# Optimization experiments

Measured on AMD Instinct MI355X. Metric: run time of the kernel, lower is better.

Reference implementation:

```python
import jax, jax.numpy as jnp
import numpy as np
import math

B, S, D, H = 2, 2048, 1024, 16
DK = D // H
EPS = 1e-5

def setup_inputs() -> dict:
    key = jax.random.key(0)
    ks = jax.random.split(key, 16)
    s = 0.02
    return {
        'query': jax.random.normal(ks[0], (B, S, D), jnp.float32),
        'key': jax.random.normal(ks[1], (B, S, D), jnp.float32),
        'value': jax.random.normal(ks[2], (B, S, D), jnp.float32),
        'mask': jax.random.randint(ks[3], (B, 1, S, S), 0, 2, jnp.int32),
        'market_context': jax.random.normal(ks[4], (B, D), jnp.float32),
        'Wq': jax.random.normal(ks[5], (D, D), jnp.float32) * s,
        'bq': jnp.zeros((D,), jnp.float32),
        'Wk': jax.random.normal(ks[6], (D, D), jnp.float32) * s,
        'bk': jnp.zeros((D,), jnp.float32),
        'Wv': jax.random.normal(ks[7], (D, D), jnp.float32) * s,
        'bv': jnp.zeros((D,), jnp.float32),
        'Wo': jax.random.normal(ks[8], (D, D), jnp.float32) * s,
        'bo': jnp.zeros((D,), jnp.float32),
        'Wc': jax.random.normal(ks[9], (D, D), jnp.float32) * s,
        'bc': jnp.zeros((D,), jnp.float32),
        'ln_g': jnp.ones((D,), jnp.float32),
        'ln_b': jnp.zeros((D,), jnp.float32),
    }

def reference(query, key, value, mask, market_context,
              Wq, bq, Wk, bk, Wv, bv, Wo, bo, Wc, bc, ln_g, ln_b):
    b, s, d = query.shape
    # QKV projections -> [B, H, S, DK]
    Q = (query @ Wq + bq).reshape(b, s, H, DK).transpose(0, 2, 1, 3)
    K = (key @ Wk + bk).reshape(b, s, H, DK).transpose(0, 2, 1, 3)
    V = (value @ Wv + bv).reshape(b, s, H, DK).transpose(0, 2, 1, 3)
    # market context -> per-head bias added to K (broadcast over sequence)
    ctx = (market_context @ Wc + bc).reshape(b, H, DK)
    K = K + ctx[:, :, None, :]
    scores = jnp.einsum('bhqd,bhkd->bhqk', Q, K) / math.sqrt(DK)
    scores = jnp.where(mask == 0, jnp.float32(-1e9), scores)
    attn = jax.nn.softmax(scores, axis=-1)  # dropout is identity in eval
    ctx2 = jnp.einsum('bhqk,bhkd->bhqd', attn, V)
    ctx2 = ctx2.transpose(0, 2, 1, 3).reshape(b, s, d)
    out = ctx2 @ Wo + bo
    x = out + query
    mu = jnp.mean(x, axis=-1, keepdims=True)
    var = jnp.mean((x - mu) ** 2, axis=-1, keepdims=True)
    return (x - mu) * jax.lax.rsqrt(var + EPS) * ln_g + ln_b
```

## Files before the change

### kernel.cpp

```cpp
#include <hip/hip_runtime.h>
#include <cstdint>

typedef unsigned short u16;
typedef __attribute__((ext_vector_type(8))) short s16x8;
typedef __attribute__((ext_vector_type(8))) unsigned short u16x8;
typedef __attribute__((ext_vector_type(4))) float f32x4;
typedef __attribute__((ext_vector_type(16))) float f32x16;
typedef __attribute__((ext_vector_type(2))) unsigned uint2v;
typedef __attribute__((ext_vector_type(4))) unsigned uint4v;

#define CKF 0.18033688011f

__device__ inline u16 f2bf(float f){
  union { float f; uint32_t u; } v; v.f = f;
  uint32_t r = v.u + 0x7fffu + ((v.u >> 16) & 1u);
  return (u16)(r >> 16);
}

__device__ inline f32x4 mfma16(s16x8 a, s16x8 b, f32x4 c){
  return __builtin_amdgcn_mfma_f32_16x16x32_bf16(a, b, c, 0, 0, 0);
}
__device__ inline f32x16 mfma32(s16x8 a, s16x8 b, f32x16 c){
  return __builtin_amdgcn_mfma_f32_32x32x16_bf16(a, b, c, 0, 0, 0);
}
__device__ inline unsigned cvtpk(float a, float b){
  unsigned r;
  asm("v_cvt_pk_bf16_f32 %0, %1, %2" : "=v"(r) : "v"(a), "v"(b));
  return r;
}
__device__ inline float exp2a(float x){
  float r;
  asm("v_exp_f32 %0, %1" : "=v"(r) : "v"(x));
  return r;
}
__device__ inline void glds16(const u16* g, u16* l){
  __builtin_amdgcn_global_load_lds((const __attribute__((address_space(1))) void*)g,
                                   (__attribute__((address_space(3))) void*)l, 16, 0, 0);
}
__device__ inline void glds4(const unsigned* g, unsigned* l){
  __builtin_amdgcn_global_load_lds((const __attribute__((address_space(1))) void*)g,
                                   (__attribute__((address_space(3))) void*)l, 4, 0, 0);
}

__global__ __launch_bounds__(256) void convert3_kernel(
    const float* __restrict__ q, const float* __restrict__ k, const float* __restrict__ v,
    u16* __restrict__ qo, u16* __restrict__ ko, u16* __restrict__ vo){
  const float* src = (blockIdx.y == 0) ? q : (blockIdx.y == 1) ? k : v;
  u16* dst = (blockIdx.y == 0) ? qo : (blockIdx.y == 1) ? ko : vo;
  size_t i = ((size_t)blockIdx.x * 256 + threadIdx.x) * 8;
  float4 a = *(const float4*)(src + i);
  float4 b = *(const float4*)(src + i + 4);
  u16x8 o = { f2bf(a.x), f2bf(a.y), f2bf(a.z), f2bf(a.w),
              f2bf(b.x), f2bf(b.y), f2bf(b.z), f2bf(b.w) };
  *(u16x8*)(dst + i) = o;
}

__global__ void transw_kernel(
    const float* __restrict__ W0, const float* __restrict__ W1,
    const float* __restrict__ W2, const float* __restrict__ W3,
    u16* __restrict__ T0, u16* __restrict__ T1, u16* __restrict__ T2, u16* __restrict__ T3){
  const float* W = (blockIdx.z == 0) ? W0 : (blockIdx.z == 1) ? W1 : (blockIdx.z == 2) ? W2 : W3;
  u16* T = (blockIdx.z == 0) ? T0 : (blockIdx.z == 1) ? T1 : (blockIdx.z == 2) ? T2 : T3;
  __shared__ float t[32][33];
  int n0 = blockIdx.x * 32, k0 = blockIdx.y * 32;
  int tx = threadIdx.x, ty = threadIdx.y;
  #pragma unroll
  for (int j = 0; j < 4; j++)
    t[ty + j*8][tx] = W[(size_t)(k0 + ty + j*8) * 1024 + n0 + tx];
  __syncthreads();
  #pragma unroll
  for (int j = 0; j < 4; j++)
    T[(size_t)(n0 + ty + j*8) * 1024 + k0 + tx] = f2bf(t[tx][ty + j*8]);
}

__global__ __launch_bounds__(256) void packmask_kernel(const int* __restrict__ mask,
                                                       unsigned* __restrict__ bits){
  size_t i = (size_t)blockIdx.x * 256 + threadIdx.x;
  int v = mask[i];
  unsigned long long bal = __ballot(v != 0);
  int lane = threadIdx.x & 63;
  if (lane == 0)       bits[i >> 5] = (unsigned)bal;
  else if (lane == 32) bits[i >> 5] = (unsigned)(bal >> 32);
}

__global__ __launch_bounds__(256) void ctx_kernel(const float* __restrict__ mc,
                                                  const float* __restrict__ Wc,
                                                  const float* __restrict__ bc,
                                                  float* __restrict__ ctx){
  int c = threadIdx.x & 63, kk = threadIdx.x >> 6;
  int col = blockIdx.x * 64 + c;
  float a0 = 0.f, a1 = 0.f;
  for (int k = kk * 256; k < kk * 256 + 256; k++){
    float wv = Wc[(size_t)k * 1024 + col];
    a0 += mc[k] * wv;
    a1 += mc[1024 + k] * wv;
  }
  __shared__ float red[2][4][64];
  red[0][kk][c] = a0; red[1][kk][c] = a1;
  __syncthreads();
  if (threadIdx.x < 64){
    int cc = threadIdx.x;
    ctx[blockIdx.x*64 + cc] = red[0][0][cc] + red[0][1][cc] + red[0][2][cc] + red[0][3][cc]
                              + bc[blockIdx.x*64 + cc];
  } else if (threadIdx.x < 128){
    int cc = threadIdx.x - 64;
    ctx[1024 + blockIdx.x*64 + cc] = red[1][0][cc] + red[1][1][cc] + red[1][2][cc] + red[1][3][cc]
                                     + bc[blockIdx.x*64 + cc];
  }
}

struct GemmParams {
  const u16* A0; const u16* A1; const u16* A2; const u16* A3;
  const u16* W0; const u16* W1; const u16* W2; const u16* W3;
  const float* b0; const float* b1; const float* b2;
  const float* ctx;
  u16* outQ; u16* outK; u16* outV; float* outX0; float* outX1;
  int which;
};

__global__ __launch_bounds__(256) void gemm_kernel(GemmParams P){
  int o = blockIdx.x + (blockIdx.y << 3) + (blockIdx.z << 8);
  int xcd = o & 7, j = o >> 3;
  int by = xcd + ((j & 3) << 3);
  int bx = (j >> 2) & 7;
  int bz = j >> 5;

  int z, kbase, nkt;
  const u16* A; const u16* W;
  if (P.which < 0){
    z = bz; kbase = 0; nkt = 32;
    if (z == 0){ A = P.A0; W = P.W0; }
    else if (z == 1){ A = P.A1; W = P.W1; }
    else { A = P.A2; W = P.W2; }
  } else {
    z = 3; kbase = bz * 512; nkt = 16;
    A = P.A3; W = P.W3;
  }
  int m0 = by * 128, n0 = bx * 128;
  __shared__ __align__(16) u16 sm[16384];
  int tid = threadIdx.x, lane = tid & 63, w = tid >> 6;
  int li = lane & 15, lq = lane >> 4;
  int wm = w >> 1, wn = w & 1;
  f32x4 zero = {0.f, 0.f, 0.f, 0.f};
  f32x4 acc[4][4];
  #pragma unroll
  for (int i = 0; i < 4; i++)
    #pragma unroll
    for (int jj = 0; jj < 4; jj++) acc[i][jj] = zero;

  int scolS = ((lane & 3) ^ ((lane >> 3) & 3)) << 3;
  int row0 = w * 16 + (lane >> 2);
  const u16* aS0 = A + (size_t)(m0 + row0) * 1024 + kbase + scolS;
  const u16* aS1 = aS0 + (size_t)64 * 1024;
  const u16* bS0 = W + (size_t)(n0 + row0) * 1024 + kbase + scolS;
  const u16* bS1 = bS0 + (size_t)64 * 1024;
  int aD0 = (w * 64) * 8, aD1 = (256 + w * 64) * 8;

  int aOff[4], bOff[4];
  #pragma unroll
  for (int mb = 0; mb < 4; mb++){
    int row = wm * 64 + mb * 16 + li;
    aOff[mb] = (row * 32 + ((lq ^ ((row >> 1) & 3)) << 3)) * 2;
  }
  #pragma unroll
  for (int nb = 0; nb < 4; nb++){
    int row = wn * 64 + nb * 16 + li;
    bOff[nb] = 8192 + (row * 32 + ((lq ^ ((row >> 1) & 3)) << 3)) * 2;
  }

  auto STAGE = [&](int ct){
    u16* Ab = &sm[ct * 8192];
    u16* Bb = &sm[ct * 8192 + 4096];
    glds16(aS0, Ab + aD0);
    glds16(aS1, Ab + aD1);
    glds16(bS0, Bb + aD0);
    glds16(bS1, Bb + aD1);
  };
  auto ADV = [&](){ aS0 += 32; aS1 += 32; bS0 += 32; bS1 += 32; };

  auto KITER = [&](int kt, int ct){
    __builtin_amdgcn_s_barrier();
    if (kt + 1 < nkt){
      STAGE(ct ^ 1); ADV();
      asm volatile("s_waitcnt vmcnt(4)" ::: "memory");
    } else {
      asm volatile("s_waitcnt vmcnt(0)" ::: "memory");
    }
    __builtin_amdgcn_sched_barrier(0);
    __builtin_amdgcn_s_barrier();
    const char* base = (const char*)sm + ct * 16384;
    s16x8 af[4], bfr[4];
    #pragma unroll
    for (int mb = 0; mb < 4; mb++) af[mb] = *(const s16x8*)(base + aOff[mb]);
    #pragma unroll
    for (int nb = 0; nb < 4; nb++) bfr[nb] = *(const s16x8*)(base + bOff[nb]);
    __builtin_amdgcn_s_setprio(1);
    #pragma unroll
    for (int mb = 0; mb < 4; mb++)
      #pragma unroll
      for (int nb = 0; nb < 4; nb++)
        acc[mb][nb] = mfma16(af[mb], bfr[nb], acc[mb][nb]);
    __builtin_amdgcn_s_setprio(0);
  };

  STAGE(0); ADV();
  for (int kt = 0; kt < nkt; kt += 2){
    KITER(kt, 0);
    KITER(kt + 1, 1);
  }

  if (z == 2){
    const float* bias = P.b2;
    __syncthreads();
    u16* Ot = sm;
    #pragma unroll
    for (int mb = 0; mb < 4; mb++){
      #pragma unroll
      for (int nb = 0; nb < 4; nb++){
        int colL = wn * 64 + nb * 16 + li;
        int rowB = wm * 64 + mb * 16 + lq * 4;
        float bcol = bias[n0 + colL];
        unsigned p01 = cvtpk(acc[mb][nb][0] + bcol, acc[mb][nb][1] + bcol);
        unsigned p23 = cvtpk(acc[mb][nb][2] + bcol, acc[mb][nb][3] + bcol);
        int ba = colL * 256 + ((rowB * 2) ^ ((colL & 7) << 4));
        *(unsigned*)((char*)Ot + ba) = p01;
        *(unsigned*)((char*)Ot + ba + 4) = p23;
      }
    }
    __syncthreads();
    int bq_ = m0 >> 11, srow0 = m0 & 2047;
    #pragma unroll
    for (int i = 0; i < 8; i++){
      int u = i * 256 + tid;
      int colL = u >> 4, sc = u & 15;
      int ba = colL * 256 + ((sc * 16) ^ ((colL & 7) << 4));
      u16x8 vv = *(const u16x8*)((char*)Ot + ba);
      *(u16x8*)(P.outV + (((size_t)(bq_ * 1024 + n0 + colL)) << 11) + srow0 + sc * 8) = vv;
    }
    return;
  }

  if (z == 3){
    float* Xo = (kbase == 0) ? P.outX0 : P.outX1;
    #pragma unroll
    for (int mb = 0; mb < 4; mb++){
      #pragma unroll
      for (int nb = 0; nb < 4; nb++){
        int col = n0 + wn * 64 + nb * 16 + li;
        #pragma unroll
        for (int r = 0; r < 4; r++){
          int row = m0 + wm * 64 + mb * 16 + lq * 4 + r;
          Xo[(size_t)row * 1024 + col] = acc[mb][nb][r];
        }
      }
    }
    return;
  }

  const float* bias = (z == 0) ? P.b0 : P.b1;
  #pragma unroll
  for (int mb = 0; mb < 4; mb++){
    #pragma unroll
    for (int nb = 0; nb < 4; nb++){
      int colL = wn * 64 + nb * 16 + li; int col = n0 + colL;
      float bcol = bias[col];
      #pragma unroll
      for (int r = 0; r < 4; r++){
        int row = m0 + wm * 64 + mb * 16 + lq * 4 + r;
        float v = acc[mb][nb][r] + bcol;
        if (z == 0){
          P.outQ[(size_t)row * 1024 + col] = f2bf(v * CKF);
        } else {
          v += P.ctx[(size_t)(row >> 11) * 1024 + col];
          P.outK[(size_t)row * 1024 + col] = f2bf(v);
        }
      }
    }
  }
}

__global__ __launch_bounds__(256) void attn_kernel(
    const u16* __restrict__ Qg, const u16* __restrict__ Kg, const u16* __restrict__ Vtg,
    const unsigned* __restrict__ mbits, u16* __restrict__ ctx2){
  __shared__ __align__(16) u16 arena[17408];
  int tid = threadIdx.x, lane = tid & 63, w = tid >> 6;
  int l31 = lane & 31, hi = lane >> 5;
  int r7 = l31 & 7;
  int orig = blockIdx.x + (blockIdx.y << 4);
  int swz = (orig & 7) * 64 + (orig >> 3);
  int q0 = (swz & 15) * 128, bh = swz >> 4, b = bh >> 4, h = bh & 15;

  s16x8 qf[4];
  {
    const u16* qp = Qg + (size_t)(b * 2048 + q0 + w * 32 + l31) * 1024 + h * 64 + hi * 8;
    #pragma unroll
    for (int ks = 0; ks < 4; ks++)
      qf[ks] = *(const s16x8*)(qp + ks * 16);
  }
  s16x8 onesf;
  #pragma unroll
  for (int e = 0; e < 8; e++) onesf[e] = (short)0x3F80;
  f32x16 ZERO;
  #pragma unroll
  for (int r = 0; r < 16; r++) ZERO[r] = 0.f;

  int scolS = ((lane & 7) ^ (lane >> 3)) << 3;
  int rowS = w * 16 + (lane >> 3);
  const u16* kS0 = Kg + (size_t)(b * 2048 + rowS) * 1024 + h * 64 + scolS;
  const u16* kS1 = kS0 + (size_t)8 * 1024;
  const u16* vS0 = Vtg + (((size_t)(bh * 64 + rowS)) << 11) + scolS;
  const u16* vS1 = vS0 + ((size_t)8 << 11);
  int um = w * 64 + lane;
  const unsigned* mS = mbits + (size_t)(b * 2048 + q0 + (um >> 1)) * 64 + (um & 1);
  int kD0 = w * 1024, kD1 = w * 1024 + 512;

  int qr = w * 32 + l31;
  int koff[2][4], voff[2][4];
  #pragma unroll
  for (int jj = 0; jj < 2; jj++)
    #pragma unroll
    for (int ks = 0; ks < 4; ks++){
      koff[jj][ks] = ((jj * 32 + l31) * 64 + (((ks * 2 + hi) ^ r7) << 3)) * 2;
      voff[jj][ks] = 8192 + ((jj * 32 + l31) * 64 + (((ks * 2 + hi) ^ r7) << 3)) * 2;
    }
  int mB = 32768 + qr * 8;

  auto STAGE = [&](int ct){
    u16* dst = &arena[ct * 8192];
    glds16(kS0, dst + kD0);
    glds16(kS1, dst + kD1);
    glds16(vS0, dst + 4096 + kD0);
    glds16(vS1, dst + 4096 + kD1);
    glds4(mS, (unsigned*)&arena[16384] + ct * 256 + w * 64);
  };
  auto ADV = [&](){
    kS0 += (size_t)64 * 1024; kS1 += (size_t)64 * 1024;
    vS0 += 64; vS1 += 64; mS += 2;
  };

  f32x16 accO[2], accS;
  #pragma unroll
  for (int d = 0; d < 2; d++) accO[d] = ZERO;
  accS = ZERO;

  STAGE(0); ADV();

  auto ITER = [&](int t, int ct){
    __builtin_amdgcn_s_barrier();
    if (t < 31){
      STAGE(ct ^ 1); ADV();
      asm volatile("s_waitcnt vmcnt(5)" ::: "memory");
    } else {
      asm volatile("s_waitcnt vmcnt(0)" ::: "memory");
    }
    __builtin_amdgcn_sched_barrier(0);
    __builtin_amdgcn_s_barrier();
    const char* base = (const char*)arena + ct * 16384;

    f32x16 S[2];
    __builtin_amdgcn_s_setprio(1);
    #pragma unroll
    for (int jj = 0; jj < 2; jj++){
      S[jj] = ZERO;
      #pragma unroll
      for (int ks = 0; ks < 4; ks++){
        s16x8 kf = *(const s16x8*)(base + koff[jj][ks]);
        S[jj] = mfma32(kf, qf[ks], S[jj]);
      }
    }
    __builtin_amdgcn_s_setprio(0);

    uint2v mw = *(const uint2v*)((const char*)arena + ct * 1024 + mB);
    unsigned mh0 = mw[0] >> (hi << 2), mh1 = mw[1] >> (hi << 2);
    #pragma unroll
    for (int jj = 0; jj < 2; jj++){
      unsigned mh = jj ? mh1 : mh0;
      #pragma unroll
      for (int rg = 0; rg < 16; rg++){
        int pos = (rg & 3) + ((rg >> 2) << 3);
        float pv = exp2a(S[jj][rg]);
        S[jj][rg] = ((mh >> pos) & 1u) ? pv : 0.f;
      }
    }

    s16x8 pf[4];
    #pragma unroll
    for (int jj = 0; jj < 2; jj++){
      #pragma unroll
      for (int hs = 0; hs < 2; hs++){
        int rb = hs * 8;
        unsigned A0 = cvtpk(S[jj][rb + 0], S[jj][rb + 1]);
        unsigned A1 = cvtpk(S[jj][rb + 2], S[jj][rb + 3]);
        unsigned B0 = cvtpk(S[jj][rb + 4], S[jj][rb + 5]);
        unsigned B1 = cvtpk(S[jj][rb + 6], S[jj][rb + 7]);
        uint2v r01 = __builtin_amdgcn_permlane32_swap(A0, B0, false, false);
        uint2v r23 = __builtin_amdgcn_permlane32_swap(A1, B1, false, false);
        uint4v uu = { r01[0], r23[0], r01[1], r23[1] };
        pf[jj * 2 + hs] = *(s16x8*)&uu;
      }
    }
    __builtin_amdgcn_s_setprio(1);
    #pragma unroll
    for (int c = 0; c < 4; c++){
      #pragma unroll
      for (int dh = 0; dh < 2; dh++){
        s16x8 vf = *(const s16x8*)(base + voff[dh][c]);
        accO[dh] = mfma32(vf, pf[c], accO[dh]);
      }
      accS = mfma32(onesf, pf[c], accS);
    }
    __builtin_amdgcn_s_setprio(0);
  };

  for (int t = 0; t < 32; t += 2){
    ITER(t, 0);
    ITER(t + 1, 1);
  }

  __syncthreads();
  float lsum = accS[0];
  float inv = 1.f / lsum;
  u16* Ot = arena;
  #pragma unroll
  for (int dh = 0; dh < 2; dh++){
    #pragma unroll
    for (int rg = 0; rg < 16; rg += 2){
      int dk = dh * 32 + (rg & 3) + ((rg >> 2) << 3) + (hi << 2);
      unsigned pk = cvtpk(accO[dh][rg] * inv, accO[dh][rg + 1] * inv);
      *(unsigned*)&Ot[qr * 64 + (((dk >> 3) ^ (qr & 7)) << 3) + (dk & 7)] = pk;
    }
  }
  __syncthreads();
  #pragma unroll
  for (int i = 0; i < 4; i++){
    int u = i * 256 + tid, row = u >> 3, slot = u & 7;
    u16x8 vv = *(const u16x8*)&Ot[row * 64 + ((slot ^ (row & 7)) << 3)];
    *(u16x8*)(ctx2 + (size_t)(b * 2048 + q0 + row) * 1024 + h * 64 + slot * 8) = vv;
  }
}

__global__ __launch_bounds__(256) void ln_kernel(const float* __restrict__ X0,
                                                 const float* __restrict__ X1,
                                                 const float* __restrict__ qres,
                                                 const float* __restrict__ bo,
                                                 const float* __restrict__ g,
                                                 const float* __restrict__ bb,
                                                 float* __restrict__ out){
  size_t row = blockIdx.x;
  int tid = threadIdx.x;
  float4 a = *(const float4*)(X0 + row * 1024 + tid * 4);
  float4 c = *(const float4*)(X1 + row * 1024 + tid * 4);
  float4 q = *(const float4*)(qres + row * 1024 + tid * 4);
  float4 bv = *(const float4*)(bo + tid * 4);
  float4 v;
  v.x = a.x + c.x + q.x + bv.x;
  v.y = a.y + c.y + q.y + bv.y;
  v.z = a.z + c.z + q.z + bv.z;
  v.w = a.w + c.w + q.w + bv.w;
  float s = v.x + v.y + v.z + v.w;
  float s2 = v.x*v.x + v.y*v.y + v.z*v.z + v.w*v.w;
  #pragma unroll
  for (int o = 1; o < 64; o <<= 1){
    s += __shfl_xor(s, o, 64);
    s2 += __shfl_xor(s2, o, 64);
  }
  __shared__ float rs[4], rs2[4];
  int w = tid >> 6;
  if ((tid & 63) == 0){ rs[w] = s; rs2[w] = s2; }
  __syncthreads();
  s = rs[0] + rs[1] + rs[2] + rs[3];
  s2 = rs2[0] + rs2[1] + rs2[2] + rs2[3];
  float mu = s * (1.f / 1024.f);
  float var = s2 * (1.f / 1024.f) - mu * mu;
  float rstd = rsqrtf(var + 1e-5f);
  float4 gg = *(const float4*)(g + tid * 4);
  float4 bt = *(const float4*)(bb + tid * 4);
  float4 o;
  o.x = (v.x - mu) * rstd * gg.x + bt.x;
  o.y = (v.y - mu) * rstd * gg.y + bt.y;
  o.z = (v.z - mu) * rstd * gg.z + bt.z;
  o.w = (v.w - mu) * rstd * gg.w + bt.w;
  *(float4*)(out + row * 1024 + tid * 4) = o;
}

extern "C" void kernel_launch(void* const* d_in, const int* in_sizes, int n_in,
                              void* d_out, int out_size, void* d_ws, size_t ws_size,
                              hipStream_t stream){
  const float* query = (const float*)d_in[0];
  const float* key_  = (const float*)d_in[1];
  const float* value = (const float*)d_in[2];
  const int*   mask  = (const int*)d_in[3];
  const float* mc    = (const float*)d_in[4];
  const float* Wq = (const float*)d_in[5];  const float* bq = (const float*)d_in[6];
  const float* Wk = (const float*)d_in[7];  const float* bk = (const float*)d_in[8];
  const float* Wv = (const float*)d_in[9];  const float* bv = (const float*)d_in[10];
  const float* Wo = (const float*)d_in[11]; const float* bo = (const float*)d_in[12];
  const float* Wc = (const float*)d_in[13]; const float* bc = (const float*)d_in[14];
  const float* lng = (const float*)d_in[15]; const float* lnb = (const float*)d_in[16];
  float* outp = (float*)d_out;
  uint8_t* ws = (uint8_t*)d_ws;
  const size_t MB = (size_t)1 << 20;
  if (ws_size < 58 * MB) return;

  u16* q_bf = (u16*)(ws + 0);
  u16* k_bf = (u16*)(ws + 8 * MB);
  u16* v_bf = (u16*)(ws + 16 * MB);
  float* X0 = (float*)(ws + 8 * MB);
  u16* Qb   = (u16*)(ws + 24 * MB);
  u16* Kb   = (u16*)(ws + 32 * MB);
  float* X1 = (float*)(ws + 32 * MB);
  u16* Vt   = (u16*)(ws + 40 * MB);
  u16* Wqt  = (u16*)(ws + 48 * MB);
  u16* Wkt  = (u16*)(ws + 50 * MB);
  u16* Wvt  = (u16*)(ws + 52 * MB);
  u16* Wot  = (u16*)(ws + 54 * MB);
  unsigned* mbits = (unsigned*)(ws + 56 * MB);
  float* ctxf = (float*)(ws + 57 * MB);
  u16* ctx2 = q_bf;

  convert3_kernel<<<dim3(2048, 3), 256, 0, stream>>>(query, key_, value, q_bf, k_bf, v_bf);
  transw_kernel<<<dim3(32, 32, 4), dim3(32, 8), 0, stream>>>(Wq, Wk, Wv, Wo, Wqt, Wkt, Wvt, Wot);
  packmask_kernel<<<32768, 256, 0, stream>>>(mask, mbits);
  ctx_kernel<<<16, 256, 0, stream>>>(mc, Wc, bc, ctxf);

  GemmParams gp;
  gp.A0 = q_bf; gp.A1 = k_bf; gp.A2 = v_bf; gp.A3 = ctx2;
  gp.W0 = Wqt;  gp.W1 = Wkt;  gp.W2 = Wvt;  gp.W3 = Wot;
  gp.b0 = bq;   gp.b1 = bk;   gp.b2 = bv;
  gp.ctx = ctxf;
  gp.outQ = Qb; gp.outK = Kb; gp.outV = Vt; gp.outX0 = X0; gp.outX1 = X1;
  gp.which = -1;
  gemm_kernel<<<dim3(8, 32, 3), 256, 0, stream>>>(gp);

  attn_kernel<<<dim3(16, 32), 256, 0, stream>>>(Qb, Kb, Vt, mbits, ctx2);

  gp.which = 3;
  gemm_kernel<<<dim3(8, 32, 2), 256, 0, stream>>>(gp);

  ln_kernel<<<4096, 256, 0, stream>>>(X0, X1, query, bo, lng, lnb, outp);
}
```

Before: 170.1 us.

## Merge prep kernels into one launch and widen GEMM tiles to 128x256

Four preprocessing kernels (input conversion, weight transpose, mask packing, context projection) are merged into a single launch that dispatches on block index, which removes three launch gaps. The GEMM tile grows from 128x128 to 128x256 with 8 accumulator fragments per wave, more shared memory and launch_bounds(256,2). The V-transpose epilogue now runs in two halves so it fits the shared buffer. This gives more operand reuse per tile, at the cost of half as many blocks (fewer than the CU count for the output projection) and higher register pressure.

```diff
diff --git a/kernel.cpp b/kernel.cpp
--- a/kernel.cpp
+++ b/kernel.cpp
@@ -42,70 +42,73 @@
                                    (__attribute__((address_space(3))) void*)l, 4, 0, 0);
 }
 
-__global__ __launch_bounds__(256) void convert3_kernel(
-    const float* __restrict__ q, const float* __restrict__ k, const float* __restrict__ v,
-    u16* __restrict__ qo, u16* __restrict__ ko, u16* __restrict__ vo){
-  const float* src = (blockIdx.y == 0) ? q : (blockIdx.y == 1) ? k : v;
-  u16* dst = (blockIdx.y == 0) ? qo : (blockIdx.y == 1) ? ko : vo;
-  size_t i = ((size_t)blockIdx.x * 256 + threadIdx.x) * 8;
-  float4 a = *(const float4*)(src + i);
-  float4 b = *(const float4*)(src + i + 4);
-  u16x8 o = { f2bf(a.x), f2bf(a.y), f2bf(a.z), f2bf(a.w),
-              f2bf(b.x), f2bf(b.y), f2bf(b.z), f2bf(b.w) };
-  *(u16x8*)(dst + i) = o;
-}
-
-__global__ void transw_kernel(
-    const float* __restrict__ W0, const float* __restrict__ W1,
-    const float* __restrict__ W2, const float* __restrict__ W3,
-    u16* __restrict__ T0, u16* __restrict__ T1, u16* __restrict__ T2, u16* __restrict__ T3){
-  const float* W = (blockIdx.z == 0) ? W0 : (blockIdx.z == 1) ? W1 : (blockIdx.z == 2) ? W2 : W3;
-  u16* T = (blockIdx.z == 0) ? T0 : (blockIdx.z == 1) ? T1 : (blockIdx.z == 2) ? T2 : T3;
-  __shared__ float t[32][33];
-  int n0 = blockIdx.x * 32, k0 = blockIdx.y * 32;
-  int tx = threadIdx.x, ty = threadIdx.y;
-  #pragma unroll
-  for (int j = 0; j < 4; j++)
-    t[ty + j*8][tx] = W[(size_t)(k0 + ty + j*8) * 1024 + n0 + tx];
-  __syncthreads();
-  #pragma unroll
-  for (int j = 0; j < 4; j++)
-    T[(size_t)(n0 + ty + j*8) * 1024 + k0 + tx] = f2bf(t[tx][ty + j*8]);
-}
-
-__global__ __launch_bounds__(256) void packmask_kernel(const int* __restrict__ mask,
-                                                       unsigned* __restrict__ bits){
-  size_t i = (size_t)blockIdx.x * 256 + threadIdx.x;
-  int v = mask[i];
-  unsigned long long bal = __ballot(v != 0);
-  int lane = threadIdx.x & 63;
-  if (lane == 0)       bits[i >> 5] = (unsigned)bal;
-  else if (lane == 32) bits[i >> 5] = (unsigned)(bal >> 32);
-}
-
-__global__ __launch_bounds__(256) void ctx_kernel(const float* __restrict__ mc,
-                                                  const float* __restrict__ Wc,
-                                                  const float* __restrict__ bc,
-                                                  float* __restrict__ ctx){
-  int c = threadIdx.x & 63, kk = threadIdx.x >> 6;
-  int col = blockIdx.x * 64 + c;
-  float a0 = 0.f, a1 = 0.f;
-  for (int k = kk * 256; k < kk * 256 + 256; k++){
-    float wv = Wc[(size_t)k * 1024 + col];
-    a0 += mc[k] * wv;
-    a1 += mc[1024 + k] * wv;
-  }
-  __shared__ float red[2][4][64];
-  red[0][kk][c] = a0; red[1][kk][c] = a1;
-  __syncthreads();
-  if (threadIdx.x < 64){
-    int cc = threadIdx.x;
-    ctx[blockIdx.x*64 + cc] = red[0][0][cc] + red[0][1][cc] + red[0][2][cc] + red[0][3][cc]
-                              + bc[blockIdx.x*64 + cc];
-  } else if (threadIdx.x < 128){
-    int cc = threadIdx.x - 64;
-    ctx[1024 + blockIdx.x*64 + cc] = red[1][0][cc] + red[1][1][cc] + red[1][2][cc] + red[1][3][cc]
-                                     + bc[blockIdx.x*64 + cc];
+struct PrepParams {
+  const float* q; const float* k; const float* v;
+  const int* mask; const float* mc;
+  const float* W0; const float* W1; const float* W2; const float* W3;
+  const float* Wc; const float* bc;
+  u16* qo; u16* ko; u16* vo;
+  u16* T0; u16* T1; u16* T2; u16* T3;
+  unsigned* bits; float* ctx;
+};
+
+__global__ __launch_bounds__(256) void prep_kernel(PrepParams PP){
+  __shared__ float shf[1056];
+  int blk = blockIdx.x, tid = threadIdx.x;
+  if (blk < 6144){
+    int byy = blk >> 11, bxx = blk & 2047;
+    const float* src = (byy == 0) ? PP.q : (byy == 1) ? PP.k : PP.v;
+    u16* dst = (byy == 0) ? PP.qo : (byy == 1) ? PP.ko : PP.vo;
+    size_t i = ((size_t)bxx * 256 + tid) * 8;
+    float4 a = *(const float4*)(src + i);
+    float4 b = *(const float4*)(src + i + 4);
+    u16x8 o = { f2bf(a.x), f2bf(a.y), f2bf(a.z), f2bf(a.w),
+                f2bf(b.x), f2bf(b.y), f2bf(b.z), f2bf(b.w) };
+    *(u16x8*)(dst + i) = o;
+  } else if (blk < 10240){
+    int idx = blk - 6144;
+    int bxx = idx & 31, byy = (idx >> 5) & 31, bzz = idx >> 10;
+    const float* W = (bzz == 0) ? PP.W0 : (bzz == 1) ? PP.W1 : (bzz == 2) ? PP.W2 : PP.W3;
+    u16* T = (bzz == 0) ? PP.T0 : (bzz == 1) ? PP.T1 : (bzz == 2) ? PP.T2 : PP.T3;
+    float (*t)[33] = (float(*)[33])shf;
+    int n0 = bxx * 32, k0 = byy * 32;
+    int tx = tid & 31, ty = tid >> 5;
+    #pragma unroll
+    for (int j = 0; j < 4; j++)
+      t[ty + j*8][tx] = W[(size_t)(k0 + ty + j*8) * 1024 + n0 + tx];
+    __syncthreads();
+    #pragma unroll
+    for (int j = 0; j < 4; j++)
+      T[(size_t)(n0 + ty + j*8) * 1024 + k0 + tx] = f2bf(t[tx][ty + j*8]);
+  } else if (blk < 43008){
+    size_t i = (size_t)(blk - 10240) * 256 + tid;
+    int v = PP.mask[i];
+    unsigned long long bal = __ballot(v != 0);
+    int lane = tid & 63;
+    if (lane == 0)       PP.bits[i >> 5] = (unsigned)bal;
+    else if (lane == 32) PP.bits[i >> 5] = (unsigned)(bal >> 32);
+  } else {
+    int cb = blk - 43008;
+    int c = tid & 63, kk = tid >> 6;
+    int col = cb * 64 + c;
+    float a0 = 0.f, a1 = 0.f;
+    for (int k = kk * 256; k < kk * 256 + 256; k++){
+      float wv = PP.Wc[(size_t)k * 1024 + col];
+      a0 += PP.mc[k] * wv;
+      a1 += PP.mc[1024 + k] * wv;
+    }
+    float* red = shf;
+    red[(0*4 + kk)*64 + c] = a0;
+    red[(1*4 + kk)*64 + c] = a1;
+    __syncthreads();
+    if (tid < 64){
+      int cc = tid;
+      PP.ctx[cb*64 + cc] = red[cc] + red[64+cc] + red[128+cc] + red[192+cc] + PP.bc[cb*64 + cc];
+    } else if (tid < 128){
+      int cc = tid - 64;
+      PP.ctx[1024 + cb*64 + cc] = red[256+cc] + red[320+cc] + red[384+cc] + red[448+cc]
+                                  + PP.bc[cb*64 + cc];
+    }
   }
 }
 
@@ -118,12 +121,12 @@
   int which;
 };
 
-__global__ __launch_bounds__(256) void gemm_kernel(GemmParams P){
-  int o = blockIdx.x + (blockIdx.y << 3) + (blockIdx.z << 8);
+__global__ __launch_bounds__(256, 2) void gemm_kernel(GemmParams P){
+  int o = blockIdx.x + (blockIdx.y << 2) + (blockIdx.z << 7);
   int xcd = o & 7, j = o >> 3;
   int by = xcd + ((j & 3) << 3);
-  int bx = (j >> 2) & 7;
-  int bz = j >> 5;
+  int bx = (j >> 2) & 3;
+  int bz = j >> 4;
 
   int z, kbase, nkt;
   const u16* A; const u16* W;
@@ -136,69 +139,74 @@
     z = 3; kbase = bz * 512; nkt = 16;
     A = P.A3; W = P.W3;
   }
-  int m0 = by * 128, n0 = bx * 128;
-  __shared__ __align__(16) u16 sm[16384];
+  int m0 = by * 128, n0 = bx * 256;
+  __shared__ __align__(16) u16 sm[24576];
   int tid = threadIdx.x, lane = tid & 63, w = tid >> 6;
   int li = lane & 15, lq = lane >> 4;
   int wm = w >> 1, wn = w & 1;
   f32x4 zero = {0.f, 0.f, 0.f, 0.f};
-  f32x4 acc[4][4];
+  f32x4 acc[4][8];
   #pragma unroll
   for (int i = 0; i < 4; i++)
     #pragma unroll
-    for (int jj = 0; jj < 4; jj++) acc[i][jj] = zero;
+    for (int jj = 0; jj < 8; jj++) acc[i][jj] = zero;
 
   int scolS = ((lane & 3) ^ ((lane >> 3) & 3)) << 3;
-  int row0 = w * 16 + (lane >> 2);
-  const u16* aS0 = A + (size_t)(m0 + row0) * 1024 + kbase + scolS;
+  int rowS = w * 16 + (lane >> 2);
+  const u16* aS0 = A + (size_t)(m0 + rowS) * 1024 + kbase + scolS;
   const u16* aS1 = aS0 + (size_t)64 * 1024;
-  const u16* bS0 = W + (size_t)(n0 + row0) * 1024 + kbase + scolS;
+  const u16* bS0 = W + (size_t)(n0 + rowS) * 1024 + kbase + scolS;
   const u16* bS1 = bS0 + (size_t)64 * 1024;
-  int aD0 = (w * 64) * 8, aD1 = (256 + w * 64) * 8;
-
-  int aOff[4], bOff[4];
+  const u16* bS2 = bS0 + (size_t)128 * 1024;
+  const u16* bS3 = bS0 + (size_t)192 * 1024;
+  int d0 = (w * 64) * 8, d1 = (256 + w * 64) * 8;
+  int d2 = (512 + w * 64) * 8, d3 = (768 + w * 64) * 8;
+
+  int aOff[4], bOff[8];
   #pragma unroll
   for (int mb = 0; mb < 4; mb++){
     int row = wm * 64 + mb * 16 + li;
     aOff[mb] = (row * 32 + ((lq ^ ((row >> 1) & 3)) << 3)) * 2;
   }
   #pragma unroll
-  for (int nb = 0; nb < 4; nb++){
-    int row = wn * 64 + nb * 16 + li;
+  for (int nb = 0; nb < 8; nb++){
+    int row = wn * 128 + nb * 16 + li;
     bOff[nb] = 8192 + (row * 32 + ((lq ^ ((row >> 1) & 3)) << 3)) * 2;
   }
 
   auto STAGE = [&](int ct){
-    u16* Ab = &sm[ct * 8192];
-    u16* Bb = &sm[ct * 8192 + 4096];
-    glds16(aS0, Ab + aD0);
-    glds16(aS1, Ab + aD1);
-    glds16(bS0, Bb + aD0);
-    glds16(bS1, Bb + aD1);
+    u16* Ab = &sm[ct * 12288];
+    u16* Bb = &sm[ct * 12288 + 4096];
+    glds16(aS0, Ab + d0);
+    glds16(aS1, Ab + d1);
+    glds16(bS0, Bb + d0);
+    glds16(bS1, Bb + d1);
+    glds16(bS2, Bb + d2);
+    glds16(bS3, Bb + d3);
   };
-  auto ADV = [&](){ aS0 += 32; aS1 += 32; bS0 += 32; bS1 += 32; };
+  auto ADV = [&](){ aS0 += 32; aS1 += 32; bS0 += 32; bS1 += 32; bS2 += 32; bS3 += 32; };
 
   auto KITER = [&](int kt, int ct){
     __builtin_amdgcn_s_barrier();
     if (kt + 1 < nkt){
       STAGE(ct ^ 1); ADV();
-      asm volatile("s_waitcnt vmcnt(4)" ::: "memory");
+      asm volatile("s_waitcnt vmcnt(6)" ::: "memory");
     } else {
       asm volatile("s_waitcnt vmcnt(0)" ::: "memory");
     }
     __builtin_amdgcn_sched_barrier(0);
     __builtin_amdgcn_s_barrier();
-    const char* base = (const char*)sm + ct * 16384;
-    s16x8 af[4], bfr[4];
+    const char* base = (const char*)sm + ct * 24576;
+    s16x8 af[4], bfr[8];
     #pragma unroll
     for (int mb = 0; mb < 4; mb++) af[mb] = *(const s16x8*)(base + aOff[mb]);
     #pragma unroll
-    for (int nb = 0; nb < 4; nb++) bfr[nb] = *(const s16x8*)(base + bOff[nb]);
+    for (int nb = 0; nb < 8; nb++) bfr[nb] = *(const s16x8*)(base + bOff[nb]);
     __builtin_amdgcn_s_setprio(1);
     #pragma unroll
     for (int mb = 0; mb < 4; mb++)
       #pragma unroll
-      for (int nb = 0; nb < 4; nb++)
+      for (int nb = 0; nb < 8; nb++)
         acc[mb][nb] = mfma16(af[mb], bfr[nb], acc[mb][nb]);
     __builtin_amdgcn_s_setprio(0);
   };
@@ -211,31 +219,36 @@
 
   if (z == 2){
     const float* bias = P.b2;
-    __syncthreads();
+    int bq_ = m0 >> 11, srow0 = m0 & 2047;
     u16* Ot = sm;
     #pragma unroll
-    for (int mb = 0; mb < 4; mb++){
-      #pragma unroll
-      for (int nb = 0; nb < 4; nb++){
-        int colL = wn * 64 + nb * 16 + li;
-        int rowB = wm * 64 + mb * 16 + lq * 4;
-        float bcol = bias[n0 + colL];
-        unsigned p01 = cvtpk(acc[mb][nb][0] + bcol, acc[mb][nb][1] + bcol);
-        unsigned p23 = cvtpk(acc[mb][nb][2] + bcol, acc[mb][nb][3] + bcol);
-        int ba = colL * 256 + ((rowB * 2) ^ ((colL & 7) << 4));
-        *(unsigned*)((char*)Ot + ba) = p01;
-        *(unsigned*)((char*)Ot + ba + 4) = p23;
-      }
-    }
-    __syncthreads();
-    int bq_ = m0 >> 11, srow0 = m0 & 2047;
-    #pragma unroll
-    for (int i = 0; i < 8; i++){
-      int u = i * 256 + tid;
-      int colL = u >> 4, sc = u & 15;
-      int ba = colL * 256 + ((sc * 16) ^ ((colL & 7) << 4));
-      u16x8 vv = *(const u16x8*)((char*)Ot + ba);
-      *(u16x8*)(P.outV + (((size_t)(bq_ * 1024 + n0 + colL)) << 11) + srow0 + sc * 8) = vv;
+    for (int h2 = 0; h2 < 2; h2++){
+      __syncthreads();
+      if (wn == h2){
+        #pragma unroll
+        for (int mb = 0; mb < 4; mb++){
+          #pragma unroll
+          for (int nb = 0; nb < 8; nb++){
+            int cl = nb * 16 + li;
+            int rowB = wm * 64 + mb * 16 + lq * 4;
+            float bcol = bias[n0 + h2 * 128 + cl];
+            unsigned p01 = cvtpk(acc[mb][nb][0] + bcol, acc[mb][nb][1] + bcol);
+            unsigned p23 = cvtpk(acc[mb][nb][2] + bcol, acc[mb][nb][3] + bcol);
+            int ba = cl * 256 + ((rowB * 2) ^ ((cl & 7) << 4));
+            *(unsigned*)((char*)Ot + ba) = p01;
+            *(unsigned*)((char*)Ot + ba + 4) = p23;
+          }
+        }
+      }
+      __syncthreads();
+      #pragma unroll
+      for (int i = 0; i < 8; i++){
+        int u = i * 256 + tid;
+        int cl = u >> 4, sc = u & 15;
+        int ba = cl * 256 + ((sc * 16) ^ ((cl & 7) << 4));
+        u16x8 vv = *(const u16x8*)((char*)Ot + ba);
+        *(u16x8*)(P.outV + (((size_t)(bq_ * 1024 + n0 + h2 * 128 + cl)) << 11) + srow0 + sc * 8) = vv;
+      }
     }
     return;
   }
@@ -245,8 +258,8 @@
     #pragma unroll
     for (int mb = 0; mb < 4; mb++){
       #pragma unroll
-      for (int nb = 0; nb < 4; nb++){
-        int col = n0 + wn * 64 + nb * 16 + li;
+      for (int nb = 0; nb < 8; nb++){
+        int col = n0 + wn * 128 + nb * 16 + li;
         #pragma unroll
         for (int r = 0; r < 4; r++){
           int row = m0 + wm * 64 + mb * 16 + lq * 4 + r;
@@ -261,8 +274,8 @@
   #pragma unroll
   for (int mb = 0; mb < 4; mb++){
     #pragma unroll
-    for (int nb = 0; nb < 4; nb++){
-      int colL = wn * 64 + nb * 16 + li; int col = n0 + colL;
+    for (int nb = 0; nb < 8; nb++){
+      int colL = wn * 128 + nb * 16 + li; int col = n0 + colL;
       float bcol = bias[col];
       #pragma unroll
       for (int r = 0; r < 4; r++){
@@ -518,10 +531,13 @@
   float* ctxf = (float*)(ws + 57 * MB);
   u16* ctx2 = q_bf;
 
-  convert3_kernel<<<dim3(2048, 3), 256, 0, stream>>>(query, key_, value, q_bf, k_bf, v_bf);
-  transw_kernel<<<dim3(32, 32, 4), dim3(32, 8), 0, stream>>>(Wq, Wk, Wv, Wo, Wqt, Wkt, Wvt, Wot);
-  packmask_kernel<<<32768, 256, 0, stream>>>(mask, mbits);
-  ctx_kernel<<<16, 256, 0, stream>>>(mc, Wc, bc, ctxf);
+  PrepParams PP;
+  PP.q = query; PP.k = key_; PP.v = value; PP.mask = mask; PP.mc = mc;
+  PP.W0 = Wq; PP.W1 = Wk; PP.W2 = Wv; PP.W3 = Wo; PP.Wc = Wc; PP.bc = bc;
+  PP.qo = q_bf; PP.ko = k_bf; PP.vo = v_bf;
+  PP.T0 = Wqt; PP.T1 = Wkt; PP.T2 = Wvt; PP.T3 = Wot;
+  PP.bits = mbits; PP.ctx = ctxf;
+  prep_kernel<<<43024, 256, 0, stream>>>(PP);
 
   GemmParams gp;
   gp.A0 = q_bf; gp.A1 = k_bf; gp.A2 = v_bf; gp.A3 = ctx2;
@@ -530,12 +546,12 @@
   gp.ctx = ctxf;
   gp.outQ = Qb; gp.outK = Kb; gp.outV = Vt; gp.outX0 = X0; gp.outX1 = X1;
   gp.which = -1;
-  gemm_kernel<<<dim3(8, 32, 3), 256, 0, stream>>>(gp);
+  gemm_kernel<<<dim3(4, 32, 3), 256, 0, stream>>>(gp);
 
   attn_kernel<<<dim3(16, 32), 256, 0, stream>>>(Qb, Kb, Vt, mbits, ctx2);
 
   gp.which = 3;
-  gemm_kernel<<<dim3(8, 32, 2), 256, 0, stream>>>(gp);
+  gemm_kernel<<<dim3(4, 32, 2), 256, 0, stream>>>(gp);
 
   ln_kernel<<<4096, 256, 0, stream>>>(X0, X1, query, bo, lng, lnb, outp);
 }
```

New measurement: 219.8 us. +29.2%, slower.
